# Optimization experiments

Hardware: AMD Instinct MI355X
Metric: run time of the kernel (lower is better)

Reference implementation:

```python
import jax, jax.numpy as jnp
import numpy as np

N = 50000          # nodes
E = 1250000        # edges (avg degree 25)
EMBED = 64
HIDS = [64, 64, 64]
EDGE_DIM = 7       # 1 + 6
VOCAB = 5 ** 8     # 390625
NEG_SLOPE = 0.01   # F.leaky_relu default


def setup_inputs() -> dict:
    key = jax.random.key(0)
    ks = jax.random.split(key, 14)
    L = len(HIDS)
    x = jax.random.randint(ks[0], (N,), 0, VOCAB)
    edge_index = jax.random.randint(ks[1], (2, E), 0, N)
    edge_attr = jax.random.normal(ks[2], (E, EDGE_DIM), dtype=jnp.float32)
    emb = jax.random.normal(ks[3], (VOCAB, EMBED), dtype=jnp.float32) * 0.02
    # all layers have in = out = 64, so params are stacked along layer axis
    lin1_w = jax.random.normal(ks[4], (L, EMBED + EDGE_DIM, HIDS[0]), dtype=jnp.float32) * 0.1
    att_l = jax.random.normal(ks[5], (L, HIDS[0]), dtype=jnp.float32) * 0.1
    att_r = jax.random.normal(ks[6], (L, EMBED), dtype=jnp.float32) * 0.1
    lin2_w = jax.random.normal(ks[7], (L, HIDS[0], HIDS[0]), dtype=jnp.float32) * 0.1
    gbias = jax.random.normal(ks[8], (L, HIDS[0]), dtype=jnp.float32) * 0.01
    d_cat = int(np.sum(HIDS)) + EMBED  # 256
    fc1_w = jax.random.normal(ks[9], (d_cat, 20), dtype=jnp.float32) * 0.05
    fc1_b = jax.random.normal(ks[10], (20,), dtype=jnp.float32) * 0.01
    fc2_w = jax.random.normal(ks[11], (20, 1), dtype=jnp.float32) * 0.1
    fc2_b = jax.random.normal(ks[12], (1,), dtype=jnp.float32) * 0.01
    return {"x": x, "edge_index": edge_index, "edge_attr": edge_attr, "emb": emb,
            "lin1_w": lin1_w, "att_l": att_l, "att_r": att_r, "lin2_w": lin2_w,
            "gbias": gbias, "fc1_w": fc1_w, "fc1_b": fc1_b, "fc2_w": fc2_w, "fc2_b": fc2_b}


def _gate_conv(h, src, dst, edge_attr, w1, al, ar, w2, b):
    # message from source j -> target i; attention softmax over edges sharing a target
    xj = jnp.concatenate([h[src], edge_attr], axis=-1)            # [E, in+7]
    xj = jax.nn.leaky_relu(xj @ w1, NEG_SLOPE)                    # [E, out]
    alpha = jax.nn.leaky_relu(jnp.sum(xj * al, -1) + jnp.sum(h[dst] * ar, -1), NEG_SLOPE)
    amax = jax.ops.segment_max(alpha, dst, num_segments=N)        # [N]
    ea = jnp.exp(alpha - amax[dst])                               # [E]
    denom = jax.ops.segment_sum(ea, dst, num_segments=N)          # [N]
    a = ea / (denom[dst] + 1e-16)
    msg = (xj @ w2) * a[:, None]                                  # [E, out]
    return jax.ops.segment_sum(msg, dst, num_segments=N) + b      # [N, out]


def reference(x, edge_index, edge_attr, emb, lin1_w, att_l, att_r, lin2_w,
              gbias, fc1_w, fc1_b, fc2_w, fc2_b):
    src, dst = edge_index[0], edge_index[1]
    h = emb[x]                                                    # [N, EMBED]
    feats = [h]
    for l in range(len(HIDS)):
        h = jax.nn.relu(_gate_conv(h, src, dst, edge_attr,
                                   lin1_w[l], att_l[l], att_r[l], lin2_w[l], gbias[l]))
        feats.append(h)
    hcat = jnp.concatenate(feats, axis=-1)                        # [N, 256]
    z = jax.nn.relu(hcat @ fc1_w + fc1_b)
    out = jax.nn.sigmoid(z @ fc2_w + fc2_b)
    return out.squeeze(-1)                                        # [N]
```

## Files before the change

### kernel.cpp

```cpp
#include <hip/hip_runtime.h>
#include <math.h>

#define NEG 0.01f

typedef _Float16 f16;
typedef f16 h2 __attribute__((ext_vector_type(2)));

__device__ __forceinline__ float lrelu(float x) { return x > 0.f ? x : NEG * x; }

__device__ __forceinline__ h2 lrelu2(h2 x) {
    h2 y = x * (f16)0.01f;
    return __builtin_elementwise_max(x, y);
}

__device__ __forceinline__ float q16_allsum(float v) {
    int x;
    x = __builtin_amdgcn_update_dpp(0, __float_as_int(v), 0xB1, 0xF, 0xF, true);  v += __int_as_float(x);
    x = __builtin_amdgcn_update_dpp(0, __float_as_int(v), 0x4E, 0xF, 0xF, true);  v += __int_as_float(x);
    x = __builtin_amdgcn_update_dpp(0, __float_as_int(v), 0x124, 0xF, 0xF, true); v += __int_as_float(x);
    x = __builtin_amdgcn_update_dpp(0, __float_as_int(v), 0x128, 0xF, 0xF, true); v += __int_as_float(x);
    return v;
}

__device__ __forceinline__ float x16_32_sum(float v) {
    v += __int_as_float(__builtin_amdgcn_ds_swizzle(__float_as_int(v), 0x401F));
    v += __shfl_xor(v, 32, 64);
    return v;
}

__global__ void k_zero(int* __restrict__ deg, int n,
                       const float* __restrict__ lin1, const float* __restrict__ attl,
                       uint4* __restrict__ wpack) {
    int i = blockIdx.x * blockDim.x + threadIdx.x;
    if (i < n) deg[i] = 0;
    if (i < 48) {
        int l = i >> 4, t = i & 15;
        const float* wb  = lin1 + (size_t)l * 71 * 64 + 64 * 64;
        const float* alp = attl + l * 64;
        unsigned int u[20];
#pragma unroll
        for (int j = 0; j < 4; j++) {
            int f = 4 * t + j;
            h2 a = { (f16)wb[f],       (f16)wb[64 + f]  }; u[j]      = __builtin_bit_cast(unsigned int, a);
            h2 b = { (f16)wb[128 + f], (f16)wb[192 + f] }; u[4 + j]  = __builtin_bit_cast(unsigned int, b);
            h2 c = { (f16)wb[256 + f], (f16)wb[320 + f] }; u[8 + j]  = __builtin_bit_cast(unsigned int, c);
            h2 d = { (f16)wb[384 + f], (f16)0.f         }; u[12 + j] = __builtin_bit_cast(unsigned int, d);
        }
        h2 e0 = { (f16)alp[4 * t],     (f16)alp[4 * t + 1] }; u[16] = __builtin_bit_cast(unsigned int, e0);
        h2 e1 = { (f16)alp[4 * t + 2], (f16)alp[4 * t + 3] }; u[17] = __builtin_bit_cast(unsigned int, e1);
        u[18] = 0; u[19] = 0;
        uint4* o = wpack + (size_t)i * 5;
        o[0] = make_uint4(u[0],  u[1],  u[2],  u[3]);
        o[1] = make_uint4(u[4],  u[5],  u[6],  u[7]);
        o[2] = make_uint4(u[8],  u[9],  u[10], u[11]);
        o[3] = make_uint4(u[12], u[13], u[14], u[15]);
        o[4] = make_uint4(u[16], u[17], u[18], u[19]);
    }
}

__global__ void k_count(const int* __restrict__ dst, int* __restrict__ deg,
                        int* __restrict__ rank, int E) {
    int e = blockIdx.x * blockDim.x + threadIdx.x;
    if (e < E) rank[e] = atomicAdd(&deg[dst[e]], 1);
}

__global__ __launch_bounds__(256) void k_scan_part(const int* __restrict__ deg,
                                                   int* __restrict__ bsum, int n) {
    __shared__ int sh[256];
    int b = blockIdx.x, t = threadIdx.x;
    int i0 = b * 1024 + t * 4;
    int s = 0;
    if (i0 + 3 < n) { int4 v = *(const int4*)(deg + i0); s = v.x + v.y + v.z + v.w; }
    else { for (int k = 0; k < 4; k++) if (i0 + k < n) s += deg[i0 + k]; }
    sh[t] = s; __syncthreads();
    for (int d = 128; d > 0; d >>= 1) { if (t < d) sh[t] += sh[t + d]; __syncthreads(); }
    if (t == 0) bsum[b] = sh[0];
}

__global__ __launch_bounds__(256) void k_scan_out(const int* __restrict__ deg,
                                                  const int* __restrict__ bsum,
                                                  int* __restrict__ off, int nb, int n) {
    __shared__ int sb[256];
    __shared__ int sh[256];
    int b = blockIdx.x, t = threadIdx.x;
    int v = (t < nb) ? bsum[t] : 0;
    sb[t] = v; __syncthreads();
    for (int d = 1; d < 256; d <<= 1) {
        int u = (t >= d) ? sb[t - d] : 0;
        __syncthreads(); sb[t] += u; __syncthreads();
    }
    int base = (b == 0) ? 0 : sb[b - 1];
    if (b == 0 && t == 0) off[n] = sb[255];
    int i0 = b * 1024 + t * 4;
    int4 v4 = make_int4(0, 0, 0, 0);
    if (i0 + 3 < n) v4 = *(const int4*)(deg + i0);
    else {
        v4.x = (i0     < n) ? deg[i0]     : 0;
        v4.y = (i0 + 1 < n) ? deg[i0 + 1] : 0;
        v4.z = (i0 + 2 < n) ? deg[i0 + 2] : 0;
        v4.w = (i0 + 3 < n) ? deg[i0 + 3] : 0;
    }
    int s = v4.x + v4.y + v4.z + v4.w;
    sh[t] = s; __syncthreads();
    for (int d = 1; d < 256; d <<= 1) {
        int u = (t >= d) ? sh[t - d] : 0;
        __syncthreads(); sh[t] += u; __syncthreads();
    }
    int ex = base + sh[t] - s;
    if (i0     < n) off[i0]     = ex;
    if (i0 + 1 < n) off[i0 + 1] = ex + v4.x;
    if (i0 + 2 < n) off[i0 + 2] = ex + v4.x + v4.y;
    if (i0 + 3 < n) off[i0 + 3] = ex + v4.x + v4.y + v4.z;
}

__global__ void k_fill_embed(const int* __restrict__ src, const int* __restrict__ dst,
                             const float* __restrict__ eattr, const int* __restrict__ off,
                             const int* __restrict__ rank, uint4* __restrict__ rec, int E,
                             int nbE,
                             const int* __restrict__ x, const float* __restrict__ emb,
                             float* __restrict__ hcat, int N) {
    if ((int)blockIdx.x < nbE) {
        int e = blockIdx.x * 256 + threadIdx.x;
        if (e >= E) return;
        int slot = off[dst[e]] + rank[e];
        const float* ap = eattr + (size_t)e * 7;
        float a0 = ap[0], a1 = ap[1], a2 = ap[2], a3 = ap[3], a4 = ap[4], a5 = ap[5], a6 = ap[6];
        uint4 rv;
        h2 p01 = { (f16)a0, (f16)a1 };
        h2 p23 = { (f16)a2, (f16)a3 };
        h2 p45 = { (f16)a4, (f16)a5 };
        rv.x = __builtin_bit_cast(unsigned int, p01);
        rv.y = __builtin_bit_cast(unsigned int, p23);
        rv.z = __builtin_bit_cast(unsigned int, p45);
        unsigned int a6b = (unsigned int)__builtin_bit_cast(unsigned short, (f16)a6);
        rv.w = a6b | ((unsigned int)src[e] << 16);
        rec[slot] = rv;
    } else {
        int idx = ((int)blockIdx.x - nbE) * 256 + threadIdx.x;
        int node = idx >> 4, j4 = (idx & 15) * 4;
        if (node < N) {
            float4 v = *(const float4*)(emb + (size_t)x[node] * 64 + j4);
            *(float4*)(hcat + (size_t)node * 256 + j4) = v;
        }
    }
}

__global__ __launch_bounds__(256) void k_gemm64(
    const float* __restrict__ A, int a_stride,
    const float* __restrict__ B, const float* __restrict__ bias,
    float* __restrict__ C, int c_stride, f16* __restrict__ Ch,
    int N, int do_relu,
    const float* __restrict__ ar, float* __restrict__ r_out)
{
    __shared__ __align__(16) float sA[64][132];
    __shared__ __align__(16) float sB[64 * 64];
    __shared__ float sar[64];
    int tid = threadIdx.x;
    int row0 = blockIdx.x * 128;

    {
        const float4* b4 = (const float4*)B;
        float4* s4 = (float4*)sB;
        for (int i = tid; i < 1024; i += 256) s4[i] = b4[i];
    }
    if (ar && tid < 64) sar[tid] = ar[tid];

#pragma unroll
    for (int pass = 0; pass < 8; ++pass) {
        int nl = pass * 16 + (tid & 15);
        int k4 = (tid >> 4) * 4;
        int n = row0 + nl; if (n >= N) n = N - 1;
        float4 v = *(const float4*)(A + (size_t)n * a_stride + k4);
        sA[k4 + 0][nl] = v.x; sA[k4 + 1][nl] = v.y;
        sA[k4 + 2][nl] = v.z; sA[k4 + 3][nl] = v.w;
    }
    __syncthreads();

    int tr = tid >> 4, tc = tid & 15;
    int r0 = tr * 8, c0 = tc * 4;
    float acc[8][4];
#pragma unroll
    for (int i = 0; i < 8; i++)
#pragma unroll
        for (int j = 0; j < 4; j++) acc[i][j] = 0.f;

#pragma unroll 4
    for (int k = 0; k < 64; ++k) {
        float4 b4 = *(const float4*)(sB + k * 64 + c0);
        float4 a0 = *(const float4*)&sA[k][r0];
        float4 a1 = *(const float4*)&sA[k][r0 + 4];
#pragma unroll
        for (int j = 0; j < 4; j++) {
            float bj = (&b4.x)[j];
            acc[0][j] += a0.x * bj; acc[1][j] += a0.y * bj;
            acc[2][j] += a0.z * bj; acc[3][j] += a0.w * bj;
            acc[4][j] += a1.x * bj; acc[5][j] += a1.y * bj;
            acc[6][j] += a1.z * bj; acc[7][j] += a1.w * bj;
        }
    }

    float4 bv = make_float4(0.f, 0.f, 0.f, 0.f);
    if (bias) bv = *(const float4*)(bias + c0);
#pragma unroll
    for (int i = 0; i < 8; i++) {
        int n = row0 + r0 + i;
        if (n < N) {
            float4 o;
            o.x = acc[i][0] + bv.x; o.y = acc[i][1] + bv.y;
            o.z = acc[i][2] + bv.z; o.w = acc[i][3] + bv.w;
            if (do_relu) {
                o.x = fmaxf(o.x, 0.f); o.y = fmaxf(o.y, 0.f);
                o.z = fmaxf(o.z, 0.f); o.w = fmaxf(o.w, 0.f);
            }
            if (C) *(float4*)(C + (size_t)n * c_stride + c0) = o;
            if (Ch) {
                uint2 gw;
                gw.x = __builtin_bit_cast(unsigned int, __builtin_amdgcn_cvt_pkrtz(o.x, o.y));
                gw.y = __builtin_bit_cast(unsigned int, __builtin_amdgcn_cvt_pkrtz(o.z, o.w));
                *(uint2*)(Ch + (size_t)n * 64 + c0) = gw;
            }
        }
    }

    if (r_out && tid < 128) {
        int n = row0 + tid;
        if (n < N) {
            float racc = 0.f;
#pragma unroll
            for (int k = 0; k < 64; k++) racc += sA[k][tid] * sar[k];
            r_out[n] = racc;
        }
    }
}

__global__ __launch_bounds__(256) void k_gemm2g1(
    float* __restrict__ hc,
    const float* __restrict__ W2, const float* __restrict__ bias,
    const float* __restrict__ W1n, const float* __restrict__ arn,
    f16* __restrict__ g, float* __restrict__ r_out, int N)
{
    __shared__ __align__(16) float sA[64][132];
    __shared__ __align__(16) float sB[64 * 64];
    __shared__ float sar[64];
    int tid = threadIdx.x, row0 = blockIdx.x * 128;

    {
        const float4* b4 = (const float4*)W2;
        float4* s4 = (float4*)sB;
        for (int i = tid; i < 1024; i += 256) s4[i] = b4[i];
    }
    if (tid < 64) sar[tid] = arn[tid];

#pragma unroll
    for (int pass = 0; pass < 8; ++pass) {
        int nl = pass * 16 + (tid & 15);
        int k4 = (tid >> 4) * 4;
        int n = row0 + nl; if (n >= N) n = N - 1;
        float4 v = *(const float4*)(hc + (size_t)n * 256 + k4);
        sA[k4 + 0][nl] = v.x; sA[k4 + 1][nl] = v.y;
        sA[k4 + 2][nl] = v.z; sA[k4 + 3][nl] = v.w;
    }
    __syncthreads();

    int tr = tid >> 4, tc = tid & 15;
    int r0 = tr * 8, c0 = tc * 4;
    float acc[8][4];
#pragma unroll
    for (int i = 0; i < 8; i++)
#pragma unroll
        for (int j = 0; j < 4; j++) acc[i][j] = 0.f;

#pragma unroll 4
    for (int k = 0; k < 64; ++k) {
        float4 b4 = *(const float4*)(sB + k * 64 + c0);
        float4 a0 = *(const float4*)&sA[k][r0];
        float4 a1 = *(const float4*)&sA[k][r0 + 4];
#pragma unroll
        for (int j = 0; j < 4; j++) {
            float bj = (&b4.x)[j];
            acc[0][j] += a0.x * bj; acc[1][j] += a0.y * bj;
            acc[2][j] += a0.z * bj; acc[3][j] += a0.w * bj;
            acc[4][j] += a1.x * bj; acc[5][j] += a1.y * bj;
            acc[6][j] += a1.z * bj; acc[7][j] += a1.w * bj;
        }
    }

    float4 bv = *(const float4*)(bias + c0);
#pragma unroll
    for (int i = 0; i < 8; i++) {
        acc[i][0] = fmaxf(acc[i][0] + bv.x, 0.f);
        acc[i][1] = fmaxf(acc[i][1] + bv.y, 0.f);
        acc[i][2] = fmaxf(acc[i][2] + bv.z, 0.f);
        acc[i][3] = fmaxf(acc[i][3] + bv.w, 0.f);
        int n = row0 + r0 + i;
        if (n < N) *(float4*)(hc + (size_t)n * 256 + c0) =
            make_float4(acc[i][0], acc[i][1], acc[i][2], acc[i][3]);
    }
    __syncthreads();

    {
        const float4* b4 = (const float4*)W1n;
        float4* s4 = (float4*)sB;
        for (int i = tid; i < 1024; i += 256) s4[i] = b4[i];
    }
#pragma unroll
    for (int i = 0; i < 8; i++)
#pragma unroll
        for (int j = 0; j < 4; j++) sA[c0 + j][r0 + i] = acc[i][j];
    __syncthreads();

#pragma unroll
    for (int i = 0; i < 8; i++)
#pragma unroll
        for (int j = 0; j < 4; j++) acc[i][j] = 0.f;

#pragma unroll 4
    for (int k = 0; k < 64; ++k) {
        float4 b4 = *(const float4*)(sB + k * 64 + c0);
        float4 a0 = *(const float4*)&sA[k][r0];
        float4 a1 = *(const float4*)&sA[k][r0 + 4];
#pragma unroll
        for (int j = 0; j < 4; j++) {
            float bj = (&b4.x)[j];
            acc[0][j] += a0.x * bj; acc[1][j] += a0.y * bj;
            acc[2][j] += a0.z * bj; acc[3][j] += a0.w * bj;
            acc[4][j] += a1.x * bj; acc[5][j] += a1.y * bj;
            acc[6][j] += a1.z * bj; acc[7][j] += a1.w * bj;
        }
    }

#pragma unroll
    for (int i = 0; i < 8; i++) {
        int n = row0 + r0 + i;
        if (n < N) {
            uint2 gw;
            gw.x = __builtin_bit_cast(unsigned int, __builtin_amdgcn_cvt_pkrtz(acc[i][0], acc[i][1]));
            gw.y = __builtin_bit_cast(unsigned int, __builtin_amdgcn_cvt_pkrtz(acc[i][2], acc[i][3]));
            *(uint2*)(g + (size_t)n * 64 + c0) = gw;
        }
    }
    if (tid < 128) {
        int n = row0 + tid;
        if (n < N) {
            float racc = 0.f;
#pragma unroll
            for (int k = 0; k < 64; k++) racc += sA[k][tid] * sar[k];
            r_out[n] = racc;
        }
    }
}

struct ConvW {
    h2 w01[4], w23[4], w45[4], w6_[4];
    h2 al01, al23;
};

__device__ __forceinline__ void edge_math(uint4 rv, uint2 gv, bool valid, float ri,
                                          const ConvW& W, float4& s, float& den) {
    h2 a01 = __builtin_bit_cast(h2, rv.x);
    h2 a23 = __builtin_bit_cast(h2, rv.y);
    h2 a45 = __builtin_bit_cast(h2, rv.z);
    h2 a6p = __builtin_bit_cast(h2, rv.w & 0xFFFFu);
    h2 g01 = __builtin_bit_cast(h2, gv.x);
    h2 g23 = __builtin_bit_cast(h2, gv.y);

    float c0 = __builtin_amdgcn_fdot2(a01, W.w01[0],
               __builtin_amdgcn_fdot2(a23, W.w23[0],
               __builtin_amdgcn_fdot2(a45, W.w45[0],
               __builtin_amdgcn_fdot2(a6p, W.w6_[0], 0.f, false), false), false), false);
    float c1 = __builtin_amdgcn_fdot2(a01, W.w01[1],
               __builtin_amdgcn_fdot2(a23, W.w23[1],
               __builtin_amdgcn_fdot2(a45, W.w45[1],
               __builtin_amdgcn_fdot2(a6p, W.w6_[1], 0.f, false), false), false), false);
    float c2 = __builtin_amdgcn_fdot2(a01, W.w01[2],
               __builtin_amdgcn_fdot2(a23, W.w23[2],
               __builtin_amdgcn_fdot2(a45, W.w45[2],
               __builtin_amdgcn_fdot2(a6p, W.w6_[2], 0.f, false), false), false), false);
    float c3 = __builtin_amdgcn_fdot2(a01, W.w01[3],
               __builtin_amdgcn_fdot2(a23, W.w23[3],
               __builtin_amdgcn_fdot2(a45, W.w45[3],
               __builtin_amdgcn_fdot2(a6p, W.w6_[3], 0.f, false), false), false), false);

    h2 x01 = lrelu2(g01 + __builtin_amdgcn_cvt_pkrtz(c0, c1));
    h2 x23 = lrelu2(g23 + __builtin_amdgcn_cvt_pkrtz(c2, c3));
    float p = __builtin_amdgcn_fdot2(x01, W.al01,
              __builtin_amdgcn_fdot2(x23, W.al23, 0.f, false), false);
    p = q16_allsum(p);
    float alpha = lrelu(p + ri);
    float w = valid ? __expf(alpha) : 0.f;
    s.x += w * (float)x01.x; s.y += w * (float)x01.y;
    s.z += w * (float)x23.x; s.w += w * (float)x23.y;
    den += w;
}

__global__ __launch_bounds__(256) void k_conv(
    const int* __restrict__ off, const uint4* __restrict__ rec,
    const f16* __restrict__ g, const float* __restrict__ r,
    const uint4* __restrict__ wpack, float* __restrict__ aggdst, int N)
{
    int lane = threadIdx.x & 63;
    int wid  = threadIdx.x >> 6;
    int node = blockIdx.x * 4 + wid;
    if (node >= N) return;
    int q = lane >> 4, l16 = lane & 15;

    ConvW W;
    {
        const uint4* wp = wpack + l16 * 5;
        uint4 v0 = wp[0], v1 = wp[1], v2 = wp[2], v3 = wp[3], v4 = wp[4];
        W.w01[0] = __builtin_bit_cast(h2, v0.x); W.w01[1] = __builtin_bit_cast(h2, v0.y);
        W.w01[2] = __builtin_bit_cast(h2, v0.z); W.w01[3] = __builtin_bit_cast(h2, v0.w);
        W.w23[0] = __builtin_bit_cast(h2, v1.x); W.w23[1] = __builtin_bit_cast(h2, v1.y);
        W.w23[2] = __builtin_bit_cast(h2, v1.z); W.w23[3] = __builtin_bit_cast(h2, v1.w);
        W.w45[0] = __builtin_bit_cast(h2, v2.x); W.w45[1] = __builtin_bit_cast(h2, v2.y);
        W.w45[2] = __builtin_bit_cast(h2, v2.z); W.w45[3] = __builtin_bit_cast(h2, v2.w);
        W.w6_[0] = __builtin_bit_cast(h2, v3.x); W.w6_[1] = __builtin_bit_cast(h2, v3.y);
        W.w6_[2] = __builtin_bit_cast(h2, v3.z); W.w6_[3] = __builtin_bit_cast(h2, v3.w);
        W.al01   = __builtin_bit_cast(h2, v4.x); W.al23   = __builtin_bit_cast(h2, v4.y);
    }

    float ri = r[node];
    int e0 = off[node], e1 = off[node + 1];

    float4 s = make_float4(0.f, 0.f, 0.f, 0.f);
    float den = 0.f;
    for (int e = e0; e < e1; e += 16) {
        int ea = e + q, eb = ea + 4, ec = ea + 8, ed = ea + 12;
        int last = e1 - 1;
        bool va = ea < e1, vb = eb < e1, vc = ec < e1, vd = ed < e1;
        uint4 ra = rec[va ? ea : last];
        uint4 rb = rec[vb ? eb : last];
        uint4 rc = rec[vc ? ec : last];
        uint4 rd = rec[vd ? ed : last];
        uint2 ga = *(const uint2*)(g + (size_t)(ra.w >> 16) * 64 + 4 * l16);
        uint2 gb = *(const uint2*)(g + (size_t)(rb.w >> 16) * 64 + 4 * l16);
        uint2 gc = *(const uint2*)(g + (size_t)(rc.w >> 16) * 64 + 4 * l16);
        uint2 gd = *(const uint2*)(g + (size_t)(rd.w >> 16) * 64 + 4 * l16);
        edge_math(ra, ga, va, ri, W, s, den);
        edge_math(rb, gb, vb, ri, W, s, den);
        edge_math(rc, gc, vc, ri, W, s, den);
        edge_math(rd, gd, vd, ri, W, s, den);
    }
    s.x = x16_32_sum(s.x); s.y = x16_32_sum(s.y);
    s.z = x16_32_sum(s.z); s.w = x16_32_sum(s.w);
    den = x16_32_sum(den);
    float inv = 1.f / (den + 1e-16f);
    if (q == 0) {
        float4 o = make_float4(s.x * inv, s.y * inv, s.z * inv, s.w * inv);
        *(float4*)(aggdst + (size_t)node * 256 + 4 * l16) = o;
    }
}

__global__ __launch_bounds__(256) void k_gemm2head(
    const float* __restrict__ hcat,
    const float* __restrict__ W2, const float* __restrict__ bias,
    const float* __restrict__ f1w, const float* __restrict__ f1b,
    const float* __restrict__ f2w, const float* __restrict__ f2b,
    float* __restrict__ out, int N)
{
    __shared__ __align__(16) float sA[64][132];
    __shared__ __align__(16) float sBW[5120];
    __shared__ float sP[128 * 20];
    int tid = threadIdx.x, row0 = blockIdx.x * 128;

    {
        const float4* b4 = (const float4*)W2;
        float4* s4 = (float4*)sBW;
        for (int i = tid; i < 1024; i += 256) s4[i] = b4[i];
    }
#pragma unroll
    for (int pass = 0; pass < 8; ++pass) {
        int nl = pass * 16 + (tid & 15);
        int k4 = (tid >> 4) * 4;
        int n = row0 + nl; if (n >= N) n = N - 1;
        float4 v = *(const float4*)(hcat + (size_t)n * 256 + 192 + k4);
        sA[k4 + 0][nl] = v.x; sA[k4 + 1][nl] = v.y;
        sA[k4 + 2][nl] = v.z; sA[k4 + 3][nl] = v.w;
    }
    __syncthreads();

    int tr = tid >> 4, tc = tid & 15;
    int r0 = tr * 8, c0 = tc * 4;
    float acc[8][4];
#pragma unroll
    for (int i = 0; i < 8; i++)
#pragma unroll
        for (int j = 0; j < 4; j++) acc[i][j] = 0.f;

#pragma unroll 4
    for (int k = 0; k < 64; ++k) {
        float4 b4 = *(const float4*)(sBW + k * 64 + c0);
        float4 a0 = *(const float4*)&sA[k][r0];
        float4 a1 = *(const float4*)&sA[k][r0 + 4];
#pragma unroll
        for (int j = 0; j < 4; j++) {
            float bj = (&b4.x)[j];
            acc[0][j] += a0.x * bj; acc[1][j] += a0.y * bj;
            acc[2][j] += a0.z * bj; acc[3][j] += a0.w * bj;
            acc[4][j] += a1.x * bj; acc[5][j] += a1.y * bj;
            acc[6][j] += a1.z * bj; acc[7][j] += a1.w * bj;
        }
    }

    float4 fw[5];
    {
        const float4* w4 = (const float4*)f1w;
#pragma unroll
        for (int i2 = 0; i2 < 5; i2++) fw[i2] = w4[tid + i2 * 256];
    }
    __syncthreads();

    float* sO = &sA[0][0];
    float4 bv = *(const float4*)(bias + c0);
#pragma unroll
    for (int i = 0; i < 8; i++) {
        acc[i][0] = fmaxf(acc[i][0] + bv.x, 0.f);
        acc[i][1] = fmaxf(acc[i][1] + bv.y, 0.f);
        acc[i][2] = fmaxf(acc[i][2] + bv.z, 0.f);
        acc[i][3] = fmaxf(acc[i][3] + bv.w, 0.f);
        int rr = r0 + i;
        sO[rr * 65 + c0 + 0] = acc[i][0];
        sO[rr * 65 + c0 + 1] = acc[i][1];
        sO[rr * 65 + c0 + 2] = acc[i][2];
        sO[rr * 65 + c0 + 3] = acc[i][3];
    }
    {
        float4* sw4 = (float4*)sBW;
#pragma unroll
        for (int i2 = 0; i2 < 5; i2++) sw4[tid + i2 * 256] = fw[i2];
    }
    __syncthreads();

    int rloc = tid & 127;
    int half = tid >> 7;
    int n = row0 + rloc;
    int nn = (n < N) ? n : N - 1;
    float z[20];
#pragma unroll
    for (int j = 0; j < 20; j++) z[j] = 0.f;
    const float4* hr = (const float4*)(hcat + (size_t)nn * 256);
    if (half == 0) {
        for (int k4 = 0; k4 < 32; k4++) {
            float4 h = hr[k4];
            const float* wr = sBW + k4 * 80;
#pragma unroll
            for (int j = 0; j < 20; j++)
                z[j] += h.x * wr[j] + h.y * wr[20 + j] + h.z * wr[40 + j] + h.w * wr[60 + j];
        }
    } else {
        for (int k4 = 32; k4 < 48; k4++) {
            float4 h = hr[k4];
            const float* wr = sBW + k4 * 80;
#pragma unroll
            for (int j = 0; j < 20; j++)
                z[j] += h.x * wr[j] + h.y * wr[20 + j] + h.z * wr[40 + j] + h.w * wr[60 + j];
        }
        for (int k = 0; k < 64; k += 2) {
            float hx = sO[rloc * 65 + k], hy = sO[rloc * 65 + k + 1];
            const float* wr = sBW + (192 + k) * 20;
#pragma unroll
            for (int j = 0; j < 20; j++)
                z[j] += hx * wr[j] + hy * wr[20 + j];
        }
#pragma unroll
        for (int j = 0; j < 20; j++) sP[rloc * 20 + j] = z[j];
    }
    __syncthreads();
    if (half == 0 && n < N) {
        float o = f2b[0];
#pragma unroll
        for (int j = 0; j < 20; j++) {
            float zj = z[j] + sP[rloc * 20 + j] + f1b[j];
            o += fmaxf(zj, 0.f) * f2w[j];
        }
        out[n] = 1.f / (1.f + __expf(-o));
    }
}

extern "C" void kernel_launch(void* const* d_in, const int* in_sizes, int n_in,
                              void* d_out, int out_size, void* d_ws, size_t ws_size,
                              hipStream_t stream) {
    const int*   x     = (const int*)d_in[0];
    const int*   eidx  = (const int*)d_in[1];
    const float* eattr = (const float*)d_in[2];
    const float* emb   = (const float*)d_in[3];
    const float* lin1  = (const float*)d_in[4];
    const float* attl  = (const float*)d_in[5];
    const float* attr_ = (const float*)d_in[6];
    const float* lin2  = (const float*)d_in[7];
    const float* gbias = (const float*)d_in[8];
    const float* f1w   = (const float*)d_in[9];
    const float* f1b   = (const float*)d_in[10];
    const float* f2w   = (const float*)d_in[11];
    const float* f2b   = (const float*)d_in[12];
    float* out = (float*)d_out;

    int N = in_sizes[0];
    int E = in_sizes[1] / 2;
    const int* src = eidx;
    const int* dst = eidx + E;

    char* p = (char*)d_ws;
    auto alloc = [&](size_t bytes) { void* q = (void*)p; p += (bytes + 255) & ~(size_t)255; return q; };
    float* hcat = (float*)alloc((size_t)N * 256 * 4);
    f16*   g    = (f16*)alloc((size_t)N * 64 * 2);
    float* r    = (float*)alloc((size_t)N * 4);
    int*   off  = (int*)alloc((size_t)(N + 1) * 4);
    int*   deg  = (int*)alloc((size_t)N * 4);
    int*   rank = (int*)alloc((size_t)E * 4);
    int*   bsum = (int*)alloc(256 * 4);
    uint4* rec  = (uint4*)alloc((size_t)E * 16);
    uint4* wpack = (uint4*)alloc((size_t)48 * 5 * 16);

    int nbs = (N + 1023) / 1024;
    int nbE = (E + 255) / 256;
    int nbEmb = (N * 16 + 255) / 256;

    k_zero<<<(N + 255) / 256, 256, 0, stream>>>(deg, N, lin1, attl, wpack);
    k_count<<<nbE, 256, 0, stream>>>(dst, deg, rank, E);
    k_scan_part<<<nbs, 256, 0, stream>>>(deg, bsum, N);
    k_scan_out<<<nbs, 256, 0, stream>>>(deg, bsum, off, nbs, N);
    k_fill_embed<<<nbE + nbEmb, 256, 0, stream>>>(src, dst, eattr, off, rank, rec, E,
                                                  nbE, x, emb, hcat, N);

    int nbg = (N + 127) / 128;
    int nbc = (N + 3) / 4;
    k_gemm64<<<nbg, 256, 0, stream>>>(hcat, 256, lin1, nullptr,
                                      nullptr, 0, g, N, 0, attr_, r);
    k_conv<<<nbc, 256, 0, stream>>>(off, rec, g, r, wpack, hcat + 64, N);
    for (int l = 0; l < 2; l++) {
        k_gemm2g1<<<nbg, 256, 0, stream>>>(hcat + 64 * (l + 1),
                                           lin2 + (size_t)l * 4096, gbias + l * 64,
                                           lin1 + (size_t)(l + 1) * 71 * 64,
                                           attr_ + (l + 1) * 64, g, r, N);
        k_conv<<<nbc, 256, 0, stream>>>(off, rec, g, r,
                                        wpack + (size_t)(l + 1) * 80,
                                        hcat + 64 * (l + 2), N);
    }
    k_gemm2head<<<nbg, 256, 0, stream>>>(hcat, lin2 + 2 * 4096, gbias + 128,
                                         f1w, f1b, f2w, f2b, out, N);
}
```

Measured before the change: 505.8 us.

## Fuse first-layer gemm into count kernel, shrink gemm tiles, prefetch edge records

The first layer's projection GEMM now runs inside the degree-count kernel as extra blocks and gathers embeddings directly, so the separate k_gemm64 launch and its read of hcat disappear. k_gemm2g1 drops from 128-row to 64-row tiles, giving twice as many blocks with less shared memory per block, which should raise occupancy. The conv loop software-pipelines the edge-record loads by fetching the next 16 records while the current gathers are processed. The costs are more register pressure in k_conv, extra B-matrix reloads across the smaller tiles, and atomics sharing a launch with GEMM blocks.

```diff
diff --git a/kernel.cpp b/kernel.cpp
--- a/kernel.cpp
+++ b/kernel.cpp
@@ -58,10 +58,81 @@
     }
 }
 
-__global__ void k_count(const int* __restrict__ dst, int* __restrict__ deg,
-                        int* __restrict__ rank, int E) {
-    int e = blockIdx.x * blockDim.x + threadIdx.x;
-    if (e < E) rank[e] = atomicAdd(&deg[dst[e]], 1);
+__global__ __launch_bounds__(256) void k_count_gemm(
+    const int* __restrict__ dst, int* __restrict__ deg, int* __restrict__ rank,
+    int E, int nbCnt,
+    const int* __restrict__ x, const float* __restrict__ emb,
+    const float* __restrict__ B, const float* __restrict__ ar,
+    f16* __restrict__ g, float* __restrict__ r_out, int N)
+{
+    __shared__ __align__(16) float sA[64][68];
+    __shared__ __align__(16) float sB[64 * 64];
+    __shared__ float sar[64];
+    if ((int)blockIdx.x < nbCnt) {
+        int e = blockIdx.x * 256 + threadIdx.x;
+        if (e < E) rank[e] = atomicAdd(&deg[dst[e]], 1);
+        return;
+    }
+    int tid = threadIdx.x;
+    int row0 = ((int)blockIdx.x - nbCnt) * 64;
+
+    {
+        const float4* b4 = (const float4*)B;
+        float4* s4 = (float4*)sB;
+        for (int i = tid; i < 1024; i += 256) s4[i] = b4[i];
+    }
+    if (tid < 64) sar[tid] = ar[tid];
+
+#pragma unroll
+    for (int pass = 0; pass < 4; ++pass) {
+        int nl = pass * 16 + (tid & 15);
+        int k4 = (tid >> 4) * 4;
+        int n = row0 + nl; if (n >= N) n = N - 1;
+        float4 v = *(const float4*)(emb + (size_t)x[n] * 64 + k4);
+        sA[k4 + 0][nl] = v.x; sA[k4 + 1][nl] = v.y;
+        sA[k4 + 2][nl] = v.z; sA[k4 + 3][nl] = v.w;
+    }
+    __syncthreads();
+
+    int tr = tid >> 4, tc = tid & 15;
+    int r0 = tr * 4, c0 = tc * 4;
+    float acc[4][4];
+#pragma unroll
+    for (int i = 0; i < 4; i++)
+#pragma unroll
+        for (int j = 0; j < 4; j++) acc[i][j] = 0.f;
+
+#pragma unroll 4
+    for (int k = 0; k < 64; ++k) {
+        float4 b4 = *(const float4*)(sB + k * 64 + c0);
+        float4 a0 = *(const float4*)&sA[k][r0];
+#pragma unroll
+        for (int j = 0; j < 4; j++) {
+            float bj = (&b4.x)[j];
+            acc[0][j] += a0.x * bj; acc[1][j] += a0.y * bj;
+            acc[2][j] += a0.z * bj; acc[3][j] += a0.w * bj;
+        }
+    }
+
+#pragma unroll
+    for (int i = 0; i < 4; i++) {
+        int n = row0 + r0 + i;
+        if (n < N) {
+            uint2 gw;
+            gw.x = __builtin_bit_cast(unsigned int, __builtin_amdgcn_cvt_pkrtz(acc[i][0], acc[i][1]));
+            gw.y = __builtin_bit_cast(unsigned int, __builtin_amdgcn_cvt_pkrtz(acc[i][2], acc[i][3]));
+            *(uint2*)(g + (size_t)n * 64 + c0) = gw;
+        }
+    }
+    if (tid < 64) {
+        int n = row0 + tid;
+        if (n < N) {
+            float racc = 0.f;
+#pragma unroll
+            for (int k = 0; k < 64; k++) racc += sA[k][tid] * sar[k];
+            r_out[n] = racc;
+        }
+    }
 }
 
 __global__ __launch_bounds__(256) void k_scan_part(const int* __restrict__ deg,
@@ -145,104 +216,16 @@
     }
 }
 
-__global__ __launch_bounds__(256) void k_gemm64(
-    const float* __restrict__ A, int a_stride,
-    const float* __restrict__ B, const float* __restrict__ bias,
-    float* __restrict__ C, int c_stride, f16* __restrict__ Ch,
-    int N, int do_relu,
-    const float* __restrict__ ar, float* __restrict__ r_out)
-{
-    __shared__ __align__(16) float sA[64][132];
-    __shared__ __align__(16) float sB[64 * 64];
-    __shared__ float sar[64];
-    int tid = threadIdx.x;
-    int row0 = blockIdx.x * 128;
-
-    {
-        const float4* b4 = (const float4*)B;
-        float4* s4 = (float4*)sB;
-        for (int i = tid; i < 1024; i += 256) s4[i] = b4[i];
-    }
-    if (ar && tid < 64) sar[tid] = ar[tid];
-
-#pragma unroll
-    for (int pass = 0; pass < 8; ++pass) {
-        int nl = pass * 16 + (tid & 15);
-        int k4 = (tid >> 4) * 4;
-        int n = row0 + nl; if (n >= N) n = N - 1;
-        float4 v = *(const float4*)(A + (size_t)n * a_stride + k4);
-        sA[k4 + 0][nl] = v.x; sA[k4 + 1][nl] = v.y;
-        sA[k4 + 2][nl] = v.z; sA[k4 + 3][nl] = v.w;
-    }
-    __syncthreads();
-
-    int tr = tid >> 4, tc = tid & 15;
-    int r0 = tr * 8, c0 = tc * 4;
-    float acc[8][4];
-#pragma unroll
-    for (int i = 0; i < 8; i++)
-#pragma unroll
-        for (int j = 0; j < 4; j++) acc[i][j] = 0.f;
-
-#pragma unroll 4
-    for (int k = 0; k < 64; ++k) {
-        float4 b4 = *(const float4*)(sB + k * 64 + c0);
-        float4 a0 = *(const float4*)&sA[k][r0];
-        float4 a1 = *(const float4*)&sA[k][r0 + 4];
-#pragma unroll
-        for (int j = 0; j < 4; j++) {
-            float bj = (&b4.x)[j];
-            acc[0][j] += a0.x * bj; acc[1][j] += a0.y * bj;
-            acc[2][j] += a0.z * bj; acc[3][j] += a0.w * bj;
-            acc[4][j] += a1.x * bj; acc[5][j] += a1.y * bj;
-            acc[6][j] += a1.z * bj; acc[7][j] += a1.w * bj;
-        }
-    }
-
-    float4 bv = make_float4(0.f, 0.f, 0.f, 0.f);
-    if (bias) bv = *(const float4*)(bias + c0);
-#pragma unroll
-    for (int i = 0; i < 8; i++) {
-        int n = row0 + r0 + i;
-        if (n < N) {
-            float4 o;
-            o.x = acc[i][0] + bv.x; o.y = acc[i][1] + bv.y;
-            o.z = acc[i][2] + bv.z; o.w = acc[i][3] + bv.w;
-            if (do_relu) {
-                o.x = fmaxf(o.x, 0.f); o.y = fmaxf(o.y, 0.f);
-                o.z = fmaxf(o.z, 0.f); o.w = fmaxf(o.w, 0.f);
-            }
-            if (C) *(float4*)(C + (size_t)n * c_stride + c0) = o;
-            if (Ch) {
-                uint2 gw;
-                gw.x = __builtin_bit_cast(unsigned int, __builtin_amdgcn_cvt_pkrtz(o.x, o.y));
-                gw.y = __builtin_bit_cast(unsigned int, __builtin_amdgcn_cvt_pkrtz(o.z, o.w));
-                *(uint2*)(Ch + (size_t)n * 64 + c0) = gw;
-            }
-        }
-    }
-
-    if (r_out && tid < 128) {
-        int n = row0 + tid;
-        if (n < N) {
-            float racc = 0.f;
-#pragma unroll
-            for (int k = 0; k < 64; k++) racc += sA[k][tid] * sar[k];
-            r_out[n] = racc;
-        }
-    }
-}
-
 __global__ __launch_bounds__(256) void k_gemm2g1(
     float* __restrict__ hc,
     const float* __restrict__ W2, const float* __restrict__ bias,
     const float* __restrict__ W1n, const float* __restrict__ arn,
     f16* __restrict__ g, float* __restrict__ r_out, int N)
 {
-    __shared__ __align__(16) float sA[64][132];
+    __shared__ __align__(16) float sA[64][68];
     __shared__ __align__(16) float sB[64 * 64];
     __shared__ float sar[64];
-    int tid = threadIdx.x, row0 = blockIdx.x * 128;
+    int tid = threadIdx.x, row0 = blockIdx.x * 64;
 
     {
         const float4* b4 = (const float4*)W2;
@@ -252,7 +235,7 @@
     if (tid < 64) sar[tid] = arn[tid];
 
 #pragma unroll
-    for (int pass = 0; pass < 8; ++pass) {
+    for (int pass = 0; pass < 4; ++pass) {
         int nl = pass * 16 + (tid & 15);
         int k4 = (tid >> 4) * 4;
         int n = row0 + nl; if (n >= N) n = N - 1;
@@ -263,10 +246,10 @@
     __syncthreads();
 
     int tr = tid >> 4, tc = tid & 15;
-    int r0 = tr * 8, c0 = tc * 4;
-    float acc[8][4];
-#pragma unroll
-    for (int i = 0; i < 8; i++)
+    int r0 = tr * 4, c0 = tc * 4;
+    float acc[4][4];
+#pragma unroll
+    for (int i = 0; i < 4; i++)
 #pragma unroll
         for (int j = 0; j < 4; j++) acc[i][j] = 0.f;
 
@@ -274,20 +257,17 @@
     for (int k = 0; k < 64; ++k) {
         float4 b4 = *(const float4*)(sB + k * 64 + c0);
         float4 a0 = *(const float4*)&sA[k][r0];
-        float4 a1 = *(const float4*)&sA[k][r0 + 4];
 #pragma unroll
         for (int j = 0; j < 4; j++) {
             float bj = (&b4.x)[j];
             acc[0][j] += a0.x * bj; acc[1][j] += a0.y * bj;
             acc[2][j] += a0.z * bj; acc[3][j] += a0.w * bj;
-            acc[4][j] += a1.x * bj; acc[5][j] += a1.y * bj;
-            acc[6][j] += a1.z * bj; acc[7][j] += a1.w * bj;
         }
     }
 
     float4 bv = *(const float4*)(bias + c0);
 #pragma unroll
-    for (int i = 0; i < 8; i++) {
+    for (int i = 0; i < 4; i++) {
         acc[i][0] = fmaxf(acc[i][0] + bv.x, 0.f);
         acc[i][1] = fmaxf(acc[i][1] + bv.y, 0.f);
         acc[i][2] = fmaxf(acc[i][2] + bv.z, 0.f);
@@ -304,13 +284,13 @@
         for (int i = tid; i < 1024; i += 256) s4[i] = b4[i];
     }
 #pragma unroll
-    for (int i = 0; i < 8; i++)
+    for (int i = 0; i < 4; i++)
 #pragma unroll
         for (int j = 0; j < 4; j++) sA[c0 + j][r0 + i] = acc[i][j];
     __syncthreads();
 
 #pragma unroll
-    for (int i = 0; i < 8; i++)
+    for (int i = 0; i < 4; i++)
 #pragma unroll
         for (int j = 0; j < 4; j++) acc[i][j] = 0.f;
 
@@ -318,19 +298,16 @@
     for (int k = 0; k < 64; ++k) {
         float4 b4 = *(const float4*)(sB + k * 64 + c0);
         float4 a0 = *(const float4*)&sA[k][r0];
-        float4 a1 = *(const float4*)&sA[k][r0 + 4];
 #pragma unroll
         for (int j = 0; j < 4; j++) {
             float bj = (&b4.x)[j];
             acc[0][j] += a0.x * bj; acc[1][j] += a0.y * bj;
             acc[2][j] += a0.z * bj; acc[3][j] += a0.w * bj;
-            acc[4][j] += a1.x * bj; acc[5][j] += a1.y * bj;
-            acc[6][j] += a1.z * bj; acc[7][j] += a1.w * bj;
-        }
-    }
-
-#pragma unroll
-    for (int i = 0; i < 8; i++) {
+        }
+    }
+
+#pragma unroll
+    for (int i = 0; i < 4; i++) {
         int n = row0 + r0 + i;
         if (n < N) {
             uint2 gw;
@@ -339,7 +316,7 @@
             *(uint2*)(g + (size_t)n * 64 + c0) = gw;
         }
     }
-    if (tid < 128) {
+    if (tid < 64) {
         int n = row0 + tid;
         if (n < N) {
             float racc = 0.f;
@@ -424,22 +401,32 @@
 
     float4 s = make_float4(0.f, 0.f, 0.f, 0.f);
     float den = 0.f;
-    for (int e = e0; e < e1; e += 16) {
-        int ea = e + q, eb = ea + 4, ec = ea + 8, ed = ea + 12;
+    if (e0 < e1) {
         int last = e1 - 1;
-        bool va = ea < e1, vb = eb < e1, vc = ec < e1, vd = ed < e1;
-        uint4 ra = rec[va ? ea : last];
-        uint4 rb = rec[vb ? eb : last];
-        uint4 rc = rec[vc ? ec : last];
-        uint4 rd = rec[vd ? ed : last];
-        uint2 ga = *(const uint2*)(g + (size_t)(ra.w >> 16) * 64 + 4 * l16);
-        uint2 gb = *(const uint2*)(g + (size_t)(rb.w >> 16) * 64 + 4 * l16);
-        uint2 gc = *(const uint2*)(g + (size_t)(rc.w >> 16) * 64 + 4 * l16);
-        uint2 gd = *(const uint2*)(g + (size_t)(rd.w >> 16) * 64 + 4 * l16);
-        edge_math(ra, ga, va, ri, W, s, den);
-        edge_math(rb, gb, vb, ri, W, s, den);
-        edge_math(rc, gc, vc, ri, W, s, den);
-        edge_math(rd, gd, vd, ri, W, s, den);
+        int ea = e0 + q, eb = ea + 4, ec = ea + 8, ed = ea + 12;
+        uint4 ra = rec[ea < e1 ? ea : last];
+        uint4 rb = rec[eb < e1 ? eb : last];
+        uint4 rc = rec[ec < e1 ? ec : last];
+        uint4 rd = rec[ed < e1 ? ed : last];
+        for (int e = e0; e < e1; e += 16) {
+            uint2 ga = *(const uint2*)(g + (size_t)(ra.w >> 16) * 64 + 4 * l16);
+            uint2 gb = *(const uint2*)(g + (size_t)(rb.w >> 16) * 64 + 4 * l16);
+            uint2 gc = *(const uint2*)(g + (size_t)(rc.w >> 16) * 64 + 4 * l16);
+            uint2 gd = *(const uint2*)(g + (size_t)(rd.w >> 16) * 64 + 4 * l16);
+            int en = e + 16;
+            int fa = en + q, fb = fa + 4, fc = fa + 8, fd = fa + 12;
+            uint4 na = rec[fa < e1 ? fa : last];
+            uint4 nb = rec[fb < e1 ? fb : last];
+            uint4 nc = rec[fc < e1 ? fc : last];
+            uint4 nd = rec[fd < e1 ? fd : last];
+            bool va = (e + q)      < e1, vb = (e + 4 + q)  < e1;
+            bool vc = (e + 8 + q)  < e1, vd = (e + 12 + q) < e1;
+            edge_math(ra, ga, va, ri, W, s, den);
+            edge_math(rb, gb, vb, ri, W, s, den);
+            edge_math(rc, gc, vc, ri, W, s, den);
+            edge_math(rd, gd, vd, ri, W, s, den);
+            ra = na; rb = nb; rc = nc; rd = nd;
+        }
     }
     s.x = x16_32_sum(s.x); s.y = x16_32_sum(s.y);
     s.z = x16_32_sum(s.z); s.w = x16_32_sum(s.w);
@@ -612,31 +599,31 @@
     uint4* rec  = (uint4*)alloc((size_t)E * 16);
     uint4* wpack = (uint4*)alloc((size_t)48 * 5 * 16);
 
-    int nbs = (N + 1023) / 1024;
-    int nbE = (E + 255) / 256;
+    int nbs   = (N + 1023) / 1024;
+    int nbE   = (E + 255) / 256;
     int nbEmb = (N * 16 + 255) / 256;
+    int nbg64 = (N + 63) / 64;
+    int nbg128 = (N + 127) / 128;
+    int nbc   = (N + 3) / 4;
 
     k_zero<<<(N + 255) / 256, 256, 0, stream>>>(deg, N, lin1, attl, wpack);
-    k_count<<<nbE, 256, 0, stream>>>(dst, deg, rank, E);
+    k_count_gemm<<<nbE + nbg64, 256, 0, stream>>>(dst, deg, rank, E, nbE,
+                                                  x, emb, lin1, attr_, g, r, N);
     k_scan_part<<<nbs, 256, 0, stream>>>(deg, bsum, N);
     k_scan_out<<<nbs, 256, 0, stream>>>(deg, bsum, off, nbs, N);
     k_fill_embed<<<nbE + nbEmb, 256, 0, stream>>>(src, dst, eattr, off, rank, rec, E,
                                                   nbE, x, emb, hcat, N);
 
-    int nbg = (N + 127) / 128;
-    int nbc = (N + 3) / 4;
-    k_gemm64<<<nbg, 256, 0, stream>>>(hcat, 256, lin1, nullptr,
-                                      nullptr, 0, g, N, 0, attr_, r);
     k_conv<<<nbc, 256, 0, stream>>>(off, rec, g, r, wpack, hcat + 64, N);
     for (int l = 0; l < 2; l++) {
-        k_gemm2g1<<<nbg, 256, 0, stream>>>(hcat + 64 * (l + 1),
-                                           lin2 + (size_t)l * 4096, gbias + l * 64,
-                                           lin1 + (size_t)(l + 1) * 71 * 64,
-                                           attr_ + (l + 1) * 64, g, r, N);
+        k_gemm2g1<<<nbg64, 256, 0, stream>>>(hcat + 64 * (l + 1),
+                                             lin2 + (size_t)l * 4096, gbias + l * 64,
+                                             lin1 + (size_t)(l + 1) * 71 * 64,
+                                             attr_ + (l + 1) * 64, g, r, N);
         k_conv<<<nbc, 256, 0, stream>>>(off, rec, g, r,
                                         wpack + (size_t)(l + 1) * 80,
                                         hcat + 64 * (l + 2), N);
     }
-    k_gemm2head<<<nbg, 256, 0, stream>>>(hcat, lin2 + 2 * 4096, gbias + 128,
-                                         f1w, f1b, f2w, f2b, out, N);
-}
+    k_gemm2head<<<nbg128, 256, 0, stream>>>(hcat, lin2 + 2 * 4096, gbias + 128,
+                                            f1w, f1b, f2w, f2b, out, N);
+}
```

Measured after the change: 493.8 us. -2.4%, faster.
